# Kernel tuning notes

Measured on AMD Instinct MI355X. Metric: run time of the kernel, lower is better.

## Reference

```python
import jax, jax.numpy as jnp
import numpy as np

DIM = 2048
N_HEADS = 16
N_KV_HEADS = 8
HEAD_DIM = DIM // N_HEADS  # 128
N_REP = N_HEADS // N_KV_HEADS  # 2
HIDDEN = 4 * DIM  # Project hidden dim
SEQ = 2048
BSZ = 2
ROPE_THETA = 10000.0
NEG_INF = -1e9


def setup_inputs() -> dict:
    key = jax.random.key(0)
    ks = jax.random.split(key, 10)
    s_in = 1.0 / np.sqrt(DIM)
    s_hid = 1.0 / np.sqrt(HIDDEN)
    x = jax.random.normal(ks[0], (BSZ, SEQ, DIM), jnp.float32)
    wq = jax.random.normal(ks[1], (DIM, N_HEADS * HEAD_DIM), jnp.float32) * s_in
    wk_w1 = jax.random.normal(ks[2], (DIM, HIDDEN), jnp.float32) * s_in
    wk_w2 = jax.random.normal(ks[3], (HIDDEN, N_KV_HEADS * HEAD_DIM), jnp.float32) * s_hid
    wk_w3 = jax.random.normal(ks[4], (DIM, HIDDEN), jnp.float32) * s_in
    wv_w1 = jax.random.normal(ks[5], (DIM, HIDDEN), jnp.float32) * s_in
    wv_w2 = jax.random.normal(ks[6], (HIDDEN, N_KV_HEADS * HEAD_DIM), jnp.float32) * s_hid
    wv_w3 = jax.random.normal(ks[7], (DIM, HIDDEN), jnp.float32) * s_in
    wo = jax.random.normal(ks[8], (N_HEADS * HEAD_DIM, DIM), jnp.float32) * s_in
    # RoPE tables: angle[t, j] = t * theta^(-2j/head_dim), j in [0, head_dim/2)
    inv_freq = 1.0 / (ROPE_THETA ** (np.arange(0, HEAD_DIM, 2, dtype=np.float64) / HEAD_DIM))
    ang = np.outer(np.arange(SEQ, dtype=np.float64), inv_freq)
    freqs_cos = jnp.asarray(np.cos(ang), jnp.float32)  # [SEQ, HEAD_DIM//2]
    freqs_sin = jnp.asarray(np.sin(ang), jnp.float32)
    # causal additive mask [1, 1, SEQ, SEQ]
    mask = jnp.triu(jnp.full((SEQ, SEQ), NEG_INF, jnp.float32), k=1)[None, None]
    return {
        "x": x, "wq": wq,
        "wk_w1": wk_w1, "wk_w2": wk_w2, "wk_w3": wk_w3,
        "wv_w1": wv_w1, "wv_w2": wv_w2, "wv_w3": wv_w3,
        "wo": wo, "freqs_cos": freqs_cos, "freqs_sin": freqs_sin,
        "mask": mask, "start_pos": 0,
    }


def _rope(x, cos, sin):
    # x: [b, s, h, d]; pairs (x[2j], x[2j+1]) rotated as complex multiply
    xr = x[..., 0::2]
    xi = x[..., 1::2]
    c = cos[None, :, None, :]
    s = sin[None, :, None, :]
    out_r = xr * c - xi * s
    out_i = xr * s + xi * c
    return jnp.stack([out_r, out_i], axis=-1).reshape(x.shape)


def _project(x, w1, w2, w3):
    # SwiGLU-style projection: w2(silu(x@w1) * (x@w3))
    return (jax.nn.silu(x @ w1) * (x @ w3)) @ w2


def reference(x, wq, wk_w1, wk_w2, wk_w3, wv_w1, wv_w2, wv_w3, wo,
              freqs_cos, freqs_sin, mask, start_pos):
    b, s, _ = x.shape
    q = (x @ wq).reshape(b, s, N_HEADS, HEAD_DIM)
    q = _rope(q, freqs_cos, freqs_sin)
    k = _project(x, wk_w1, wk_w2, wk_w3).reshape(b, s, N_KV_HEADS, HEAD_DIM)
    v = _project(x, wv_w1, wv_w2, wv_w3).reshape(b, s, N_KV_HEADS, HEAD_DIM)
    k = _rope(k, freqs_cos, freqs_sin)
    o_keys, o_values = k, v  # is_training=True path: cache is just current k/v
    # repeat_kv (GQA) -> [b, h, s, d]
    kr = jnp.repeat(k, N_REP, axis=2).transpose(0, 2, 1, 3)
    vr = jnp.repeat(v, N_REP, axis=2).transpose(0, 2, 1, 3)
    qt = q.transpose(0, 2, 1, 3)
    scores = jnp.einsum('bhqd,bhkd->bhqk', qt, kr) / np.sqrt(HEAD_DIM).astype(np.float32)
    scores = scores + mask
    attn = jax.nn.softmax(scores.astype(jnp.float32), axis=-1).astype(qt.dtype)
    out = jnp.einsum('bhqk,bhkd->bhqd', attn, vr)
    out = out.transpose(0, 2, 1, 3).reshape(b, s, N_HEADS * HEAD_DIM)
    return (out @ wo, o_keys, o_values)
```

## Files before the change

kernel.cpp:

```cpp
#include <hip/hip_runtime.h>

typedef unsigned short ushort_t;
typedef __attribute__((ext_vector_type(4))) float f32x4;
typedef __attribute__((ext_vector_type(8))) __bf16 bf16x8;
typedef __attribute__((ext_vector_type(4))) unsigned short ushort4_t;
typedef __attribute__((ext_vector_type(8))) unsigned short ushort8_t;
typedef __attribute__((ext_vector_type(2))) unsigned int u32x2;

#define AS1 __attribute__((address_space(1)))
#define AS3 __attribute__((address_space(3)))

__device__ __forceinline__ float bf2f(ushort_t u) {
  unsigned int v = ((unsigned int)u) << 16;
  return __builtin_bit_cast(float, v);
}
__device__ __forceinline__ ushort_t f2bf(float f) {
  unsigned int u = __builtin_bit_cast(unsigned int, f);
  u += 0x7fffu + ((u >> 16) & 1u);
  return (ushort_t)(u >> 16);
}
__device__ __forceinline__ void storeC(float* p, float v) { *p = v; }
__device__ __forceinline__ void storeC(ushort_t* p, float v) { *p = f2bf(v); }

__global__ __launch_bounds__(256) void cast_f32_bf16(const float* __restrict__ in,
                                                     ushort_t* __restrict__ outp) {
  size_t i = ((size_t)blockIdx.x * 256 + threadIdx.x) * 4;
  f32x4 v = *(const f32x4*)(const void*)&in[i];
  ushort4_t o;
#pragma unroll
  for (int j = 0; j < 4; ++j) o[j] = f2bf(v[j]);
  *(ushort4_t*)(void*)&outp[i] = o;
}

__global__ __launch_bounds__(256) void transpose_cast_b(
    const float* __restrict__ W0, const float* __restrict__ W1,
    const float* __restrict__ W2, const float* __restrict__ W3,
    ushort_t* __restrict__ Wt, int K, int N, long long strT) {
  __shared__ float tile[32][33];
  const int z = blockIdx.z;
  const float* W = (z == 0) ? W0 : (z == 1) ? W1 : (z == 2) ? W2 : W3;
  ushort_t* out = Wt + (size_t)(strT * z);
  int n0 = blockIdx.x * 32, k0 = blockIdx.y * 32;
  int tx = threadIdx.x, ty = threadIdx.y;
#pragma unroll
  for (int i = 0; i < 4; ++i)
    tile[ty + 8 * i][tx] = W[(size_t)(k0 + ty + 8 * i) * N + n0 + tx];
  __syncthreads();
#pragma unroll
  for (int i = 0; i < 4; ++i)
    out[(size_t)(n0 + ty + 8 * i) * K + k0 + tx] = f2bf(tile[tx][ty + 8 * i]);
}

__global__ __launch_bounds__(256) void silu_mul(ushort_t* __restrict__ h1,
                                                const ushort_t* __restrict__ h3) {
  size_t i = ((size_t)blockIdx.x * 256 + threadIdx.x) * 8;
  ushort8_t a = *(const ushort8_t*)(const void*)&h1[i];
  ushort8_t b = *(const ushort8_t*)(const void*)&h3[i];
#pragma unroll
  for (int j = 0; j < 8; ++j) {
    float x = bf2f(a[j]);
    float g = x / (1.0f + __expf(-x));
    a[j] = f2bf(g * bf2f(b[j]));
  }
  *(ushort8_t*)(void*)&h1[i] = a;
}

__global__ __launch_bounds__(256) void reduce_q(const float* __restrict__ part,
                                                ushort_t* __restrict__ qb,
                                                const float* __restrict__ fc,
                                                const float* __restrict__ fs) {
  const float alpha = 0.08838834764831845f;
  int p = blockIdx.x * 256 + threadIdx.x;
  int i = p & 63;
  int h = (p >> 6) & 15;
  int row = p >> 10;
  int s = row & 2047;
  size_t src = (size_t)row * 2048 + h * 128 + 2 * i;
  float xr = part[src] + part[src + 8388608];
  float xi = part[src + 1] + part[src + 8388609];
  float c = fc[s * 64 + i] * alpha, sn = fs[s * 64 + i] * alpha;
  qb[src] = f2bf(xr * c - xi * sn);
  qb[src + 1] = f2bf(xr * sn + xi * c);
}

__global__ __launch_bounds__(256) void reduce_k(const float* __restrict__ part,
                                                ushort_t* __restrict__ kb,
                                                float* __restrict__ okeys,
                                                const float* __restrict__ fc,
                                                const float* __restrict__ fs) {
  int p = blockIdx.x * 256 + threadIdx.x;
  int i = p & 63;
  int kh = (p >> 6) & 7;
  int row = p >> 9;
  int s = row & 2047;
  size_t src = (size_t)row * 1024 + kh * 128 + 2 * i;
  float xr = part[src] + part[src + 4194304] + part[src + 8388608] + part[src + 12582912];
  float xi = part[src + 1] + part[src + 1 + 4194304] + part[src + 1 + 8388608] +
             part[src + 1 + 12582912];
  float c = fc[s * 64 + i], sn = fs[s * 64 + i];
  float orr = xr * c - xi * sn;
  float oi = xr * sn + xi * c;
  kb[src] = f2bf(orr);
  kb[src + 1] = f2bf(oi);
  okeys[src] = orr;
  okeys[src + 1] = oi;
}

__global__ __launch_bounds__(256) void reduce_v(const float* __restrict__ part,
                                                float* __restrict__ ovals,
                                                ushort_t* __restrict__ vbT) {
  __shared__ ushort_t tile[32][33];
  int s0 = blockIdx.x * 32, d0 = blockIdx.y * 32, bk = blockIdx.z;
  int b = bk >> 3, kh = bk & 7;
  int tx = threadIdx.x, ty = threadIdx.y;
#pragma unroll
  for (int i = 0; i < 4; ++i) {
    int s = s0 + ty + 8 * i;
    size_t src = ((size_t)(b * 2048 + s)) * 1024 + kh * 128 + d0 + tx;
    float v = part[src] + part[src + 4194304] + part[src + 8388608] + part[src + 12582912];
    tile[ty + 8 * i][tx] = f2bf(v);
    ovals[src] = v;
  }
  __syncthreads();
#pragma unroll
  for (int i = 0; i < 4; ++i) {
    int d = d0 + ty + 8 * i;
    vbT[((size_t)bk * 128 + d) * 2048 + s0 + tx] = tile[tx][ty + 8 * i];
  }
}

__global__ __launch_bounds__(256) void reduce_wo(const float* __restrict__ part,
                                                 float* __restrict__ outp) {
  size_t i = ((size_t)blockIdx.x * 256 + threadIdx.x) * 4;
  f32x4 a = *(const f32x4*)(const void*)&part[i];
  f32x4 b = *(const f32x4*)(const void*)&part[i + 8388608];
  *(f32x4*)(void*)&outp[i] = a + b;
}

__global__ __launch_bounds__(256) void flash_attn(
    const ushort_t* __restrict__ Q, const ushort_t* __restrict__ Kg,
    const ushort_t* __restrict__ VT, ushort_t* __restrict__ O) {
  __shared__ __align__(16) char smem[81920];
  const int xp = blockIdx.x;
  const int bh = blockIdx.y;
  const int b = bh >> 4, h = bh & 15, kh = h >> 1;
  const int t = threadIdx.x, w = t >> 6, lane = t & 63;
  const int fr = lane & 15, fh = lane >> 4;
  const size_t kelem0 = ((size_t)b * 2048) * 1024 + kh * 128;
  const size_t velem0 = ((size_t)(b * 8 + kh)) * 128 * 2048;
  const size_t qrow0 = (size_t)b * 2048;

  size_t oK[4], oV[4];
#pragma unroll
  for (int qv = 0; qv < 4; ++qv) {
    int row = w * 16 + qv * 4 + (lane >> 4);
    oK[qv] = (size_t)row * 1024 + (((lane & 15) ^ (row & 7)) * 8);
    int rd = w * 32 + qv * 8 + (lane >> 3);
    oV[qv] = (size_t)rd * 2048 + (((lane & 7) ^ (rd & 7)) * 8);
  }

  auto stage = [&](int tile, int buf) {
    const size_t kc = (size_t)tile * 64 * 1024;
    const int vc = tile * 64;
    char* kd = smem + buf * 16384 + w * 4096;
    char* vd = smem + 32768 + buf * 16384 + w * 4096;
#pragma unroll
    for (int qv = 0; qv < 4; ++qv) {
      __builtin_amdgcn_global_load_lds((const AS1 void*)(Kg + kelem0 + kc + oK[qv]),
                                       (AS3 void*)(kd + qv * 1024), 16, 0, 0);
      __builtin_amdgcn_global_load_lds((const AS1 void*)(VT + velem0 + oV[qv] + vc),
                                       (AS3 void*)(vd + qv * 1024), 16, 0, 0);
    }
  };

#pragma unroll 1
  for (int ph = 0; ph < 2; ++ph) {
    const int qi = ph ? (15 - xp) : xp;
    const int qw = qi * 128 + w * 32;
    const int nt = 2 * qi + 2;

    bf16x8 qF[2][4];
#pragma unroll
    for (int qt = 0; qt < 2; ++qt)
#pragma unroll
      for (int i = 0; i < 4; ++i)
        qF[qt][i] = *(const bf16x8*)(const void*)(
            Q + (qrow0 + qw + qt * 16 + fr) * 2048 + h * 128 + i * 32 + fh * 8);

    f32x4 acco[8][2] = {};
    float mrun[2] = {-1e30f, -1e30f};
    float lrun[2] = {0.0f, 0.0f};

    stage(0, 0);
#pragma unroll 1
    for (int tt = 0; tt < nt; ++tt) {
      const int c0 = tt * 64;
      if (tt + 1 < nt) {
        stage(tt + 1, (tt + 1) & 1);
        asm volatile("s_waitcnt vmcnt(8)" ::: "memory");
      } else {
        asm volatile("s_waitcnt vmcnt(0)" ::: "memory");
      }
      __builtin_amdgcn_sched_barrier(0);
      __builtin_amdgcn_s_barrier();
      const char* KL = smem + (tt & 1) * 16384;
      const char* VL = smem + 32768 + (tt & 1) * 16384;
      char* PL = smem + 65536 + w * 4096;
      if (c0 <= qw + 31) {
        f32x4 sacc[2][4] = {};
#pragma unroll
        for (int i = 0; i < 4; ++i)
#pragma unroll
          for (int mt = 0; mt < 4; ++mt) {
            bf16x8 kf = *(const bf16x8*)(const void*)(
                KL + (mt * 16 + fr) * 256 + (((i * 4 + fh) ^ (fr & 7)) * 16));
            sacc[0][mt] = __builtin_amdgcn_mfma_f32_16x16x32_bf16(kf, qF[0][i], sacc[0][mt], 0, 0, 0);
            sacc[1][mt] = __builtin_amdgcn_mfma_f32_16x16x32_bf16(kf, qF[1][i], sacc[1][mt], 0, 0, 0);
          }
        if (c0 + 63 > qw) {
#pragma unroll
          for (int qt = 0; qt < 2; ++qt) {
            int qg = qw + qt * 16 + fr;
#pragma unroll
            for (int mt = 0; mt < 4; ++mt)
#pragma unroll
              for (int j = 0; j < 4; ++j)
                if (c0 + mt * 16 + fh * 4 + j > qg) sacc[qt][mt][j] = -1e30f;
          }
        }
#pragma unroll
        for (int qt = 0; qt < 2; ++qt) {
          float mt_ = -1e30f;
#pragma unroll
          for (int mt = 0; mt < 4; ++mt)
#pragma unroll
            for (int j = 0; j < 4; ++j) mt_ = fmaxf(mt_, sacc[qt][mt][j]);
          mt_ = fmaxf(mt_, __shfl_xor(mt_, 16, 64));
          mt_ = fmaxf(mt_, __shfl_xor(mt_, 32, 64));
          float mnew = fmaxf(mrun[qt], mt_);
          float corr = __expf(mrun[qt] - mnew);
          mrun[qt] = mnew;
          float ps = 0.0f;
          float pv[4][4];
#pragma unroll
          for (int mt = 0; mt < 4; ++mt)
#pragma unroll
            for (int j = 0; j < 4; ++j) {
              float pe = __expf(sacc[qt][mt][j] - mnew);
              pv[mt][j] = pe;
              ps += pe;
            }
          ps += __shfl_xor(ps, 16, 64);
          ps += __shfl_xor(ps, 32, 64);
          lrun[qt] = lrun[qt] * corr + ps;
#pragma unroll
          for (int mt = 0; mt < 4; ++mt) {
            unsigned int u0, u1;
            asm("v_cvt_pk_bf16_f32 %0, %1, %2" : "=v"(u0) : "v"(pv[mt][0]), "v"(pv[mt][1]));
            asm("v_cvt_pk_bf16_f32 %0, %1, %2" : "=v"(u1) : "v"(pv[mt][2]), "v"(pv[mt][3]));
            u32x2 val;
            val[0] = u0;
            val[1] = u1;
            *(u32x2*)(void*)(PL + qt * 2048 + fr * 128 +
                             (((2 * mt + (fh >> 1)) ^ (fr & 7)) * 16) + (fh & 1) * 8) = val;
          }
#pragma unroll
          for (int dt = 0; dt < 8; ++dt) acco[dt][qt] *= corr;
        }
        bf16x8 pf[2][2];
#pragma unroll
        for (int qt = 0; qt < 2; ++qt)
#pragma unroll
          for (int ks = 0; ks < 2; ++ks)
            pf[qt][ks] = *(const bf16x8*)(const void*)(
                PL + qt * 2048 + fr * 128 + (((ks * 4 + fh) ^ (fr & 7)) * 16));
#pragma unroll
        for (int dt = 0; dt < 8; ++dt)
#pragma unroll
          for (int ks = 0; ks < 2; ++ks) {
            bf16x8 vf = *(const bf16x8*)(const void*)(
                VL + (dt * 16 + fr) * 128 + (((ks * 4 + fh) ^ (fr & 7)) * 16));
            acco[dt][0] = __builtin_amdgcn_mfma_f32_16x16x32_bf16(vf, pf[0][ks], acco[dt][0], 0, 0, 0);
            acco[dt][1] = __builtin_amdgcn_mfma_f32_16x16x32_bf16(vf, pf[1][ks], acco[dt][1], 0, 0, 0);
          }
      }
      __builtin_amdgcn_s_barrier();
    }
#pragma unroll
    for (int qt = 0; qt < 2; ++qt) {
      float inv = 1.0f / lrun[qt];
      const size_t rb = (qrow0 + qw + qt * 16 + fr) * 2048 + h * 128;
#pragma unroll
      for (int dt = 0; dt < 8; ++dt) {
        ushort4_t o4;
#pragma unroll
        for (int j = 0; j < 4; ++j) o4[j] = f2bf(acco[dt][qt][j] * inv);
        *(ushort4_t*)(void*)(O + rb + dt * 16 + fh * 4) = o4;
      }
    }
  }
}

template <typename CT>
__global__ __launch_bounds__(512, 2) void gemm256(
    const ushort_t* __restrict__ A, const ushort_t* __restrict__ B,
    CT* __restrict__ C, int K, int lda, int ldb, int ldc,
    int nwgx, int nwg, long long strA, long long strB, long long strC) {
  __shared__ __align__(16) char smem[131072];
  const int bz = blockIdx.y;
  const int bid = blockIdx.x;
  const int swz = (bid & 7) * (nwg >> 3) + (bid >> 3);
  const int r0 = (swz / nwgx) * 256;
  const int c0 = (swz % nwgx) * 256;
  const int t = threadIdx.x, w = t >> 6, lane = t & 63;
  const int wm = w >> 2, wn = w & 3;
  const int fr = lane & 15, fh = lane >> 4;
  const int sl0 = (fh ^ (fr & 7)) << 4;
  const int ldsw = w * 1024;
  const int srow = t >> 3;
  const int scb = (t & 7) ^ (srow & 7);
  const int NT = K >> 6;
  const ushort_t* gA = A + strA * bz + (size_t)(r0 + srow) * lda + scb * 8;
  const ushort_t* gB = B + strB * bz + (size_t)(c0 + srow) * ldb + scb * 8;

  auto stage = [&](int tile, int isB, int h) {
    const ushort_t* g = isB ? gB : gA;
    const size_t ld = isB ? (size_t)ldb : (size_t)lda;
    char* lp = (char*)smem + ((tile & 1) << 16) + (isB ? 32768 : 0) + (h << 14) + ldsw;
    const ushort_t* src = g + (size_t)(h * 128) * ld + tile * 64;
    __builtin_amdgcn_global_load_lds((const AS1 void*)src, (AS3 void*)lp, 16, 0, 0);
    __builtin_amdgcn_global_load_lds((const AS1 void*)(src + 64 * ld),
                                     (AS3 void*)(lp + 8192), 16, 0, 0);
  };

  f32x4 acc[8][4] = {};

  stage(0, 0, 0); stage(0, 0, 1); stage(0, 1, 0); stage(0, 1, 1);
  if (NT > 1) {
    stage(1, 0, 0); stage(1, 0, 1); stage(1, 1, 0); stage(1, 1, 1);
    asm volatile("s_waitcnt vmcnt(8)" ::: "memory");
  } else {
    asm volatile("s_waitcnt vmcnt(0)" ::: "memory");
  }
  __builtin_amdgcn_sched_barrier(0);
  __builtin_amdgcn_s_barrier();

  const int aOff = wm * 16384 + fr * 128;
  const int bOff = 32768 + wn * 8192 + fr * 128;

  for (int kt = 0; kt < NT; ++kt) {
    const int buf = (kt & 1) << 16;
    const char* la = (const char*)smem + buf + aOff;
    const char* lb = (const char*)smem + buf + bOff;
    bf16x8 aF0[8], aF1[8], bF0[4], bF1[4];
#pragma unroll
    for (int m = 0; m < 8; ++m)
      aF0[m] = *(const bf16x8*)(const void*)(la + m * 2048 + sl0);
#pragma unroll
    for (int n = 0; n < 4; ++n)
      bF0[n] = *(const bf16x8*)(const void*)(lb + n * 2048 + sl0);
    __builtin_amdgcn_s_barrier();
    asm volatile("s_waitcnt lgkmcnt(0)" ::: "memory");
    __builtin_amdgcn_sched_barrier(0);
    __builtin_amdgcn_s_setprio(1);
#pragma unroll
    for (int m = 0; m < 4; ++m)
#pragma unroll
      for (int n = 0; n < 4; ++n)
        acc[m][n] = __builtin_amdgcn_mfma_f32_16x16x32_bf16(aF0[m], bF0[n], acc[m][n], 0, 0, 0);
    __builtin_amdgcn_s_setprio(0);
    __builtin_amdgcn_s_barrier();
#pragma unroll
    for (int m = 0; m < 8; ++m)
      aF1[m] = *(const bf16x8*)(const void*)(la + m * 2048 + (sl0 ^ 64));
#pragma unroll
    for (int n = 0; n < 4; ++n)
      bF1[n] = *(const bf16x8*)(const void*)(lb + n * 2048 + (sl0 ^ 64));
    __builtin_amdgcn_s_barrier();
    asm volatile("s_waitcnt lgkmcnt(0)" ::: "memory");
    __builtin_amdgcn_sched_barrier(0);
    __builtin_amdgcn_s_setprio(1);
#pragma unroll
    for (int m = 4; m < 8; ++m)
#pragma unroll
      for (int n = 0; n < 4; ++n)
        acc[m][n] = __builtin_amdgcn_mfma_f32_16x16x32_bf16(aF0[m], bF0[n], acc[m][n], 0, 0, 0);
    __builtin_amdgcn_s_setprio(0);
    __builtin_amdgcn_s_barrier();
    if (kt + 2 < NT) { stage(kt + 2, 0, 0); stage(kt + 2, 1, 0); }
    __builtin_amdgcn_s_barrier();
    __builtin_amdgcn_s_setprio(1);
#pragma unroll
    for (int m = 0; m < 4; ++m)
#pragma unroll
      for (int n = 0; n < 4; ++n)
        acc[m][n] = __builtin_amdgcn_mfma_f32_16x16x32_bf16(aF1[m], bF1[n], acc[m][n], 0, 0, 0);
    __builtin_amdgcn_s_setprio(0);
    __builtin_amdgcn_s_barrier();
    if (kt + 2 < NT) { stage(kt + 2, 0, 1); stage(kt + 2, 1, 1); }
    __builtin_amdgcn_s_setprio(1);
#pragma unroll
    for (int m = 4; m < 8; ++m)
#pragma unroll
      for (int n = 0; n < 4; ++n)
        acc[m][n] = __builtin_amdgcn_mfma_f32_16x16x32_bf16(aF1[m], bF1[n], acc[m][n], 0, 0, 0);
    __builtin_amdgcn_s_setprio(0);
    if (kt + 2 < NT)
      asm volatile("s_waitcnt vmcnt(8)" ::: "memory");
    else if (kt + 1 < NT)
      asm volatile("s_waitcnt vmcnt(0)" ::: "memory");
    __builtin_amdgcn_sched_barrier(0);
    __builtin_amdgcn_s_barrier();
  }

  CT* gC = C + strC * bz;
  const int cr = r0 + wm * 128 + fh * 4;
  const int cc = c0 + wn * 64 + fr;
#pragma unroll
  for (int m = 0; m < 8; ++m)
#pragma unroll
    for (int n = 0; n < 4; ++n)
#pragma unroll
      for (int j = 0; j < 4; ++j)
        storeC(&gC[(size_t)(cr + m * 16 + j) * ldc + cc + n * 16], acc[m][n][j]);
}

extern "C" void kernel_launch(void* const* d_in, const int* in_sizes, int n_in,
                              void* d_out, int out_size, void* d_ws, size_t ws_size,
                              hipStream_t stream) {
  const float* x = (const float*)d_in[0];
  const float* wq = (const float*)d_in[1];
  const float* wk1 = (const float*)d_in[2];
  const float* wk2 = (const float*)d_in[3];
  const float* wk3 = (const float*)d_in[4];
  const float* wv1 = (const float*)d_in[5];
  const float* wv2 = (const float*)d_in[6];
  const float* wv3 = (const float*)d_in[7];
  const float* wo = (const float*)d_in[8];
  const float* fc = (const float*)d_in[9];
  const float* fs = (const float*)d_in[10];

  float* outp = (float*)d_out;
  float* okeys = outp + 8388608;
  float* ovals = outp + 12582912;

  char* p = (char*)d_ws;
  auto alloc = [&](size_t bytes) {
    char* r = p;
    p += (bytes + 255) & ~(size_t)255;
    return r;
  };
  ushort_t* xb = (ushort_t*)alloc(8388608ull * 2);
  ushort_t* w4T = (ushort_t*)alloc(4ull * 16777216 * 2);
  ushort_t* w2T = (ushort_t*)alloc(2ull * 8388608 * 2);
  ushort_t* wqoT = (ushort_t*)alloc(2ull * 4194304 * 2);
  ushort_t* qb = (ushort_t*)alloc(8388608ull * 2);
  ushort_t* kb = (ushort_t*)alloc(4194304ull * 2);
  ushort_t* vbT = (ushort_t*)alloc(4194304ull * 2);
  ushort_t* ob = (ushort_t*)alloc(8388608ull * 2);
  char* hreg = alloc(134217728ull);
  ushort_t* h1 = (ushort_t*)hreg;
  float* part67 = (float*)(hreg + 67108864);
  float* partQO = (float*)hreg;

  ushort_t* wk1T = w4T;
  ushort_t* wk2T = w2T;
  ushort_t* wv1T = w4T + 2ull * 16777216;
  ushort_t* wv2T = w2T + 8388608;
  ushort_t* wqT = wqoT;
  ushort_t* woT = wqoT + 4194304;

  dim3 tb(32, 8);

  cast_f32_bf16<<<8192, 256, 0, stream>>>(x, xb);
  transpose_cast_b<<<dim3(256, 64, 4), tb, 0, stream>>>(wk1, wk3, wv1, wv3, w4T,
                                                        2048, 8192, 16777216);
  transpose_cast_b<<<dim3(32, 256, 2), tb, 0, stream>>>(wk2, wv2, wk2, wv2, w2T,
                                                        8192, 1024, 8388608);
  transpose_cast_b<<<dim3(64, 64, 2), tb, 0, stream>>>(wq, wo, wq, wo, wqoT,
                                                       2048, 2048, 4194304);

  gemm256<float><<<dim3(128, 2), 512, 0, stream>>>(
      xb, wqT, partQO, 1024, 2048, 2048, 2048, 8, 128, 1024, 1024, 8388608);
  reduce_q<<<16384, 256, 0, stream>>>(partQO, qb, fc, fs);

  gemm256<ushort_t><<<dim3(512, 2), 512, 0, stream>>>(
      xb, wk1T, h1, 2048, 2048, 2048, 8192, 32, 512, 0, 16777216, 33554432);
  silu_mul<<<16384, 256, 0, stream>>>(h1, h1 + 33554432);
  gemm256<float><<<dim3(64, 4), 512, 0, stream>>>(
      h1, wk2T, part67, 2048, 8192, 8192, 1024, 4, 64, 2048, 2048, 4194304);
  reduce_k<<<8192, 256, 0, stream>>>(part67, kb, okeys, fc, fs);

  gemm256<ushort_t><<<dim3(512, 2), 512, 0, stream>>>(
      xb, wv1T, h1, 2048, 2048, 2048, 8192, 32, 512, 0, 16777216, 33554432);
  silu_mul<<<16384, 256, 0, stream>>>(h1, h1 + 33554432);
  gemm256<float><<<dim3(64, 4), 512, 0, stream>>>(
      h1, wv2T, part67, 2048, 8192, 8192, 1024, 4, 64, 2048, 2048, 4194304);
  reduce_v<<<dim3(64, 4, 16), tb, 0, stream>>>(part67, ovals, vbT);

  flash_attn<<<dim3(8, 32), 256, 0, stream>>>(qb, kb, vbT, ob);

  gemm256<float><<<dim3(128, 2), 512, 0, stream>>>(
      ob, woT, partQO, 1024, 2048, 2048, 2048, 8, 128, 1024, 1024, 8388608);
  reduce_wo<<<8192, 256, 0, stream>>>(partQO, outp);

  (void)in_sizes; (void)n_in; (void)out_size; (void)ws_size;
}
```

Measured before the change: 1.048 ms.

## Rework GEMM main loop to 8-slot ring with K=32 tiles; store split-K partials in bf16

The gemm256 main loop now uses K-tiles of 32 in an 8-slot LDS ring buffer with three tiles prefetched ahead, and one barrier per iteration in place of several. Separately, the split-K partial outputs for Q, K and V are written in bf16 instead of fp32, and the reduce kernels are vectorised to process 8 elements per thread. This is meant to cut synchronisation overhead in the GEMM and halve the partial-sum memory traffic. In exchange, rounding each partial to bf16 before summing loses precision in q, k and v, and in the keys and values returned as fp32 outputs.

```diff
diff --git a/kernel.cpp b/kernel.cpp
--- a/kernel.cpp
+++ b/kernel.cpp
@@ -65,48 +65,67 @@
   *(ushort8_t*)(void*)&h1[i] = a;
 }
 
-__global__ __launch_bounds__(256) void reduce_q(const float* __restrict__ part,
+__global__ __launch_bounds__(256) void reduce_q(const ushort_t* __restrict__ part,
                                                 ushort_t* __restrict__ qb,
                                                 const float* __restrict__ fc,
                                                 const float* __restrict__ fs) {
   const float alpha = 0.08838834764831845f;
   int p = blockIdx.x * 256 + threadIdx.x;
-  int i = p & 63;
-  int h = (p >> 6) & 15;
-  int row = p >> 10;
-  int s = row & 2047;
-  size_t src = (size_t)row * 2048 + h * 128 + 2 * i;
-  float xr = part[src] + part[src + 8388608];
-  float xi = part[src + 1] + part[src + 8388609];
-  float c = fc[s * 64 + i] * alpha, sn = fs[s * 64 + i] * alpha;
-  qb[src] = f2bf(xr * c - xi * sn);
-  qb[src + 1] = f2bf(xr * sn + xi * c);
-}
-
-__global__ __launch_bounds__(256) void reduce_k(const float* __restrict__ part,
+  size_t e0 = (size_t)p * 8;
+  int i0 = (int)((e0 & 127) >> 1);
+  int s = (int)((e0 >> 11) & 2047);
+  ushort8_t a = *(const ushort8_t*)(const void*)&part[e0];
+  ushort8_t b = *(const ushort8_t*)(const void*)&part[e0 + 8388608];
+  f32x4 c4 = *(const f32x4*)(const void*)&fc[s * 64 + i0];
+  f32x4 s4 = *(const f32x4*)(const void*)&fs[s * 64 + i0];
+  ushort8_t o;
+#pragma unroll
+  for (int j = 0; j < 4; ++j) {
+    float xr = bf2f(a[2 * j]) + bf2f(b[2 * j]);
+    float xi = bf2f(a[2 * j + 1]) + bf2f(b[2 * j + 1]);
+    float c = c4[j] * alpha, sn = s4[j] * alpha;
+    o[2 * j] = f2bf(xr * c - xi * sn);
+    o[2 * j + 1] = f2bf(xr * sn + xi * c);
+  }
+  *(ushort8_t*)(void*)&qb[e0] = o;
+}
+
+__global__ __launch_bounds__(256) void reduce_k(const ushort_t* __restrict__ part,
                                                 ushort_t* __restrict__ kb,
                                                 float* __restrict__ okeys,
                                                 const float* __restrict__ fc,
                                                 const float* __restrict__ fs) {
   int p = blockIdx.x * 256 + threadIdx.x;
-  int i = p & 63;
-  int kh = (p >> 6) & 7;
-  int row = p >> 9;
-  int s = row & 2047;
-  size_t src = (size_t)row * 1024 + kh * 128 + 2 * i;
-  float xr = part[src] + part[src + 4194304] + part[src + 8388608] + part[src + 12582912];
-  float xi = part[src + 1] + part[src + 1 + 4194304] + part[src + 1 + 8388608] +
-             part[src + 1 + 12582912];
-  float c = fc[s * 64 + i], sn = fs[s * 64 + i];
-  float orr = xr * c - xi * sn;
-  float oi = xr * sn + xi * c;
-  kb[src] = f2bf(orr);
-  kb[src + 1] = f2bf(oi);
-  okeys[src] = orr;
-  okeys[src + 1] = oi;
-}
-
-__global__ __launch_bounds__(256) void reduce_v(const float* __restrict__ part,
+  size_t e0 = (size_t)p * 8;
+  int i0 = (int)((e0 & 127) >> 1);
+  int s = (int)((e0 >> 10) & 2047);
+  ushort8_t a0 = *(const ushort8_t*)(const void*)&part[e0];
+  ushort8_t a1 = *(const ushort8_t*)(const void*)&part[e0 + 4194304];
+  ushort8_t a2 = *(const ushort8_t*)(const void*)&part[e0 + 8388608];
+  ushort8_t a3 = *(const ushort8_t*)(const void*)&part[e0 + 12582912];
+  f32x4 c4 = *(const f32x4*)(const void*)&fc[s * 64 + i0];
+  f32x4 s4 = *(const f32x4*)(const void*)&fs[s * 64 + i0];
+  ushort8_t o;
+  f32x4 ov0, ov1;
+#pragma unroll
+  for (int j = 0; j < 4; ++j) {
+    float xr = bf2f(a0[2 * j]) + bf2f(a1[2 * j]) + bf2f(a2[2 * j]) + bf2f(a3[2 * j]);
+    float xi = bf2f(a0[2 * j + 1]) + bf2f(a1[2 * j + 1]) + bf2f(a2[2 * j + 1]) +
+               bf2f(a3[2 * j + 1]);
+    float c = c4[j], sn = s4[j];
+    float orr = xr * c - xi * sn;
+    float oi = xr * sn + xi * c;
+    o[2 * j] = f2bf(orr);
+    o[2 * j + 1] = f2bf(oi);
+    if (j < 2) { ov0[2 * j] = orr; ov0[2 * j + 1] = oi; }
+    else       { ov1[2 * (j - 2)] = orr; ov1[2 * (j - 2) + 1] = oi; }
+  }
+  *(ushort8_t*)(void*)&kb[e0] = o;
+  *(f32x4*)(void*)&okeys[e0] = ov0;
+  *(f32x4*)(void*)&okeys[e0 + 4] = ov1;
+}
+
+__global__ __launch_bounds__(256) void reduce_v(const ushort_t* __restrict__ part,
                                                 float* __restrict__ ovals,
                                                 ushort_t* __restrict__ vbT) {
   __shared__ ushort_t tile[32][33];
@@ -117,7 +136,8 @@
   for (int i = 0; i < 4; ++i) {
     int s = s0 + ty + 8 * i;
     size_t src = ((size_t)(b * 2048 + s)) * 1024 + kh * 128 + d0 + tx;
-    float v = part[src] + part[src + 4194304] + part[src + 8388608] + part[src + 12582912];
+    float v = bf2f(part[src]) + bf2f(part[src + 4194304]) +
+              bf2f(part[src + 8388608]) + bf2f(part[src + 12582912]);
     tile[ty + 8 * i][tx] = f2bf(v);
     ovals[src] = v;
   }
@@ -315,102 +335,86 @@
   const int t = threadIdx.x, w = t >> 6, lane = t & 63;
   const int wm = w >> 2, wn = w & 3;
   const int fr = lane & 15, fh = lane >> 4;
-  const int sl0 = (fh ^ (fr & 7)) << 4;
+  const int sl2 = (fh ^ ((fr >> 1) & 3)) << 4;
   const int ldsw = w * 1024;
-  const int srow = t >> 3;
-  const int scb = (t & 7) ^ (srow & 7);
-  const int NT = K >> 6;
+  const int srow = t >> 2;
+  const int scb = (t & 3) ^ ((srow >> 1) & 3);
+  const int NT = K >> 5;
   const ushort_t* gA = A + strA * bz + (size_t)(r0 + srow) * lda + scb * 8;
   const ushort_t* gB = B + strB * bz + (size_t)(c0 + srow) * ldb + scb * 8;
 
-  auto stage = [&](int tile, int isB, int h) {
-    const ushort_t* g = isB ? gB : gA;
-    const size_t ld = isB ? (size_t)ldb : (size_t)lda;
-    char* lp = (char*)smem + ((tile & 1) << 16) + (isB ? 32768 : 0) + (h << 14) + ldsw;
-    const ushort_t* src = g + (size_t)(h * 128) * ld + tile * 64;
-    __builtin_amdgcn_global_load_lds((const AS1 void*)src, (AS3 void*)lp, 16, 0, 0);
-    __builtin_amdgcn_global_load_lds((const AS1 void*)(src + 64 * ld),
-                                     (AS3 void*)(lp + 8192), 16, 0, 0);
+  auto stage = [&](int tile, int h, int slot) {
+    char* lp = (char*)smem + slot * 16384 + ldsw;
+    __builtin_amdgcn_global_load_lds(
+        (const AS1 void*)(gA + (size_t)(h * 128) * lda + tile * 32),
+        (AS3 void*)lp, 16, 0, 0);
+    __builtin_amdgcn_global_load_lds(
+        (const AS1 void*)(gB + (size_t)(h * 128) * ldb + tile * 32),
+        (AS3 void*)(lp + 8192), 16, 0, 0);
   };
 
   f32x4 acc[8][4] = {};
 
-  stage(0, 0, 0); stage(0, 0, 1); stage(0, 1, 0); stage(0, 1, 1);
-  if (NT > 1) {
-    stage(1, 0, 0); stage(1, 0, 1); stage(1, 1, 0); stage(1, 1, 1);
+  stage(0, 0, 0); stage(0, 1, 1);
+  if (NT > 1) { stage(1, 0, 2); stage(1, 1, 3); }
+  if (NT > 2) { stage(2, 0, 4); stage(2, 1, 5); }
+  if (NT > 2)
     asm volatile("s_waitcnt vmcnt(8)" ::: "memory");
-  } else {
+  else if (NT > 1)
+    asm volatile("s_waitcnt vmcnt(4)" ::: "memory");
+  else
     asm volatile("s_waitcnt vmcnt(0)" ::: "memory");
-  }
   __builtin_amdgcn_sched_barrier(0);
   __builtin_amdgcn_s_barrier();
-
-  const int aOff = wm * 16384 + fr * 128;
-  const int bOff = 32768 + wn * 8192 + fr * 128;
+  __builtin_amdgcn_sched_barrier(0);
+
+  int slA = wm;
+  int slB = wn >> 1;
+  int st0 = 6, st1 = 7;
+  const int bQuart = 8192 + (wn & 1) * 4096;
 
   for (int kt = 0; kt < NT; ++kt) {
-    const int buf = (kt & 1) << 16;
-    const char* la = (const char*)smem + buf + aOff;
-    const char* lb = (const char*)smem + buf + bOff;
-    bf16x8 aF0[8], aF1[8], bF0[4], bF1[4];
-#pragma unroll
-    for (int m = 0; m < 8; ++m)
-      aF0[m] = *(const bf16x8*)(const void*)(la + m * 2048 + sl0);
+    const char* la = (const char*)smem + slA * 16384 + fr * 64 + sl2;
+    const char* lb = (const char*)smem + slB * 16384 + bQuart + fr * 64 + sl2;
+    bf16x8 aF[8], bF[4];
+#pragma unroll
+    for (int m = 0; m < 4; ++m)
+      aF[m] = *(const bf16x8*)(const void*)(la + m * 1024);
 #pragma unroll
     for (int n = 0; n < 4; ++n)
-      bF0[n] = *(const bf16x8*)(const void*)(lb + n * 2048 + sl0);
-    __builtin_amdgcn_s_barrier();
-    asm volatile("s_waitcnt lgkmcnt(0)" ::: "memory");
+      bF[n] = *(const bf16x8*)(const void*)(lb + n * 1024);
+#pragma unroll
+    for (int m = 4; m < 8; ++m)
+      aF[m] = *(const bf16x8*)(const void*)(la + m * 1024);
+    if (kt + 3 < NT) { stage(kt + 3, 0, st0); stage(kt + 3, 1, st1); }
     __builtin_amdgcn_sched_barrier(0);
     __builtin_amdgcn_s_setprio(1);
 #pragma unroll
     for (int m = 0; m < 4; ++m)
 #pragma unroll
       for (int n = 0; n < 4; ++n)
-        acc[m][n] = __builtin_amdgcn_mfma_f32_16x16x32_bf16(aF0[m], bF0[n], acc[m][n], 0, 0, 0);
+        acc[m][n] = __builtin_amdgcn_mfma_f32_16x16x32_bf16(aF[m], bF[n], acc[m][n], 0, 0, 0);
+#pragma unroll
+    for (int m = 4; m < 8; ++m)
+#pragma unroll
+      for (int n = 0; n < 4; ++n)
+        acc[m][n] = __builtin_amdgcn_mfma_f32_16x16x32_bf16(aF[m], bF[n], acc[m][n], 0, 0, 0);
     __builtin_amdgcn_s_setprio(0);
-    __builtin_amdgcn_s_barrier();
-#pragma unroll
-    for (int m = 0; m < 8; ++m)
-      aF1[m] = *(const bf16x8*)(const void*)(la + m * 2048 + (sl0 ^ 64));
-#pragma unroll
-    for (int n = 0; n < 4; ++n)
-      bF1[n] = *(const bf16x8*)(const void*)(lb + n * 2048 + (sl0 ^ 64));
-    __builtin_amdgcn_s_barrier();
-    asm volatile("s_waitcnt lgkmcnt(0)" ::: "memory");
-    __builtin_amdgcn_sched_barrier(0);
-    __builtin_amdgcn_s_setprio(1);
-#pragma unroll
-    for (int m = 4; m < 8; ++m)
-#pragma unroll
-      for (int n = 0; n < 4; ++n)
-        acc[m][n] = __builtin_amdgcn_mfma_f32_16x16x32_bf16(aF0[m], bF0[n], acc[m][n], 0, 0, 0);
-    __builtin_amdgcn_s_setprio(0);
-    __builtin_amdgcn_s_barrier();
-    if (kt + 2 < NT) { stage(kt + 2, 0, 0); stage(kt + 2, 1, 0); }
-    __builtin_amdgcn_s_barrier();
-    __builtin_amdgcn_s_setprio(1);
-#pragma unroll
-    for (int m = 0; m < 4; ++m)
-#pragma unroll
-      for (int n = 0; n < 4; ++n)
-        acc[m][n] = __builtin_amdgcn_mfma_f32_16x16x32_bf16(aF1[m], bF1[n], acc[m][n], 0, 0, 0);
-    __builtin_amdgcn_s_setprio(0);
-    __builtin_amdgcn_s_barrier();
-    if (kt + 2 < NT) { stage(kt + 2, 0, 1); stage(kt + 2, 1, 1); }
-    __builtin_amdgcn_s_setprio(1);
-#pragma unroll
-    for (int m = 4; m < 8; ++m)
-#pragma unroll
-      for (int n = 0; n < 4; ++n)
-        acc[m][n] = __builtin_amdgcn_mfma_f32_16x16x32_bf16(aF1[m], bF1[n], acc[m][n], 0, 0, 0);
-    __builtin_amdgcn_s_setprio(0);
-    if (kt + 2 < NT)
-      asm volatile("s_waitcnt vmcnt(8)" ::: "memory");
-    else if (kt + 1 < NT)
-      asm volatile("s_waitcnt vmcnt(0)" ::: "memory");
-    __builtin_amdgcn_sched_barrier(0);
-    __builtin_amdgcn_s_barrier();
+    if (kt + 1 < NT) {
+      if (kt + 3 < NT)
+        asm volatile("s_waitcnt vmcnt(8)" ::: "memory");
+      else if (kt + 2 < NT)
+        asm volatile("s_waitcnt vmcnt(4)" ::: "memory");
+      else
+        asm volatile("s_waitcnt vmcnt(0)" ::: "memory");
+      __builtin_amdgcn_sched_barrier(0);
+      __builtin_amdgcn_s_barrier();
+      __builtin_amdgcn_sched_barrier(0);
+    }
+    slA = (slA + 2) & 7;
+    slB = (slB + 2) & 7;
+    st0 = (st0 + 2) & 7;
+    st1 = (st1 + 2) & 7;
   }
 
   CT* gC = C + strC * bz;
@@ -460,8 +464,9 @@
   ushort_t* ob = (ushort_t*)alloc(8388608ull * 2);
   char* hreg = alloc(134217728ull);
   ushort_t* h1 = (ushort_t*)hreg;
-  float* part67 = (float*)(hreg + 67108864);
-  float* partQO = (float*)hreg;
+  ushort_t* part16 = (ushort_t*)(hreg + 67108864);
+  ushort_t* partQ16 = (ushort_t*)hreg;
+  float* partWO = (float*)hreg;
 
   ushort_t* wk1T = w4T;
   ushort_t* wk2T = w2T;
@@ -480,29 +485,29 @@
   transpose_cast_b<<<dim3(64, 64, 2), tb, 0, stream>>>(wq, wo, wq, wo, wqoT,
                                                        2048, 2048, 4194304);
 
-  gemm256<float><<<dim3(128, 2), 512, 0, stream>>>(
-      xb, wqT, partQO, 1024, 2048, 2048, 2048, 8, 128, 1024, 1024, 8388608);
-  reduce_q<<<16384, 256, 0, stream>>>(partQO, qb, fc, fs);
+  gemm256<ushort_t><<<dim3(128, 2), 512, 0, stream>>>(
+      xb, wqT, partQ16, 1024, 2048, 2048, 2048, 8, 128, 1024, 1024, 8388608);
+  reduce_q<<<4096, 256, 0, stream>>>(partQ16, qb, fc, fs);
 
   gemm256<ushort_t><<<dim3(512, 2), 512, 0, stream>>>(
       xb, wk1T, h1, 2048, 2048, 2048, 8192, 32, 512, 0, 16777216, 33554432);
   silu_mul<<<16384, 256, 0, stream>>>(h1, h1 + 33554432);
-  gemm256<float><<<dim3(64, 4), 512, 0, stream>>>(
-      h1, wk2T, part67, 2048, 8192, 8192, 1024, 4, 64, 2048, 2048, 4194304);
-  reduce_k<<<8192, 256, 0, stream>>>(part67, kb, okeys, fc, fs);
+  gemm256<ushort_t><<<dim3(64, 4), 512, 0, stream>>>(
+      h1, wk2T, part16, 2048, 8192, 8192, 1024, 4, 64, 2048, 2048, 4194304);
+  reduce_k<<<2048, 256, 0, stream>>>(part16, kb, okeys, fc, fs);
 
   gemm256<ushort_t><<<dim3(512, 2), 512, 0, stream>>>(
       xb, wv1T, h1, 2048, 2048, 2048, 8192, 32, 512, 0, 16777216, 33554432);
   silu_mul<<<16384, 256, 0, stream>>>(h1, h1 + 33554432);
-  gemm256<float><<<dim3(64, 4), 512, 0, stream>>>(
-      h1, wv2T, part67, 2048, 8192, 8192, 1024, 4, 64, 2048, 2048, 4194304);
-  reduce_v<<<dim3(64, 4, 16), tb, 0, stream>>>(part67, ovals, vbT);
+  gemm256<ushort_t><<<dim3(64, 4), 512, 0, stream>>>(
+      h1, wv2T, part16, 2048, 8192, 8192, 1024, 4, 64, 2048, 2048, 4194304);
+  reduce_v<<<dim3(64, 4, 16), tb, 0, stream>>>(part16, ovals, vbT);
 
   flash_attn<<<dim3(8, 32), 256, 0, stream>>>(qb, kb, vbT, ob);
 
   gemm256<float><<<dim3(128, 2), 512, 0, stream>>>(
-      ob, woT, partQO, 1024, 2048, 2048, 2048, 8, 128, 1024, 1024, 8388608);
-  reduce_wo<<<8192, 256, 0, stream>>>(partQO, outp);
+      ob, woT, partWO, 1024, 2048, 2048, 2048, 8, 128, 1024, 1024, 8388608);
+  reduce_wo<<<8192, 256, 0, stream>>>(partWO, outp);
 
   (void)in_sizes; (void)n_in; (void)out_size; (void)ws_size;
 }
```

Result: faster. 1.017 ms (-3.0%).
